# Performance work log

Hardware: AMD Instinct MI355X
Metric: run time of the kernel (lower is better)

## Reference

```python
import jax, jax.numpy as jnp
import numpy as np
import math

B, S, D = 2, 2048, 2048
H, HK = 32, 8          # query heads, kv heads
HD = D // H            # 64
REP = H // HK          # 4


def setup_inputs() -> dict:
    key = jax.random.key(0)
    ks = jax.random.split(key, 6)
    x = jax.random.normal(ks[0], (B, S, D), jnp.float32)
    # RoPE tables, rotate_half convention: halves duplicated along last dim
    inv_freq = 1.0 / (10000.0 ** (jnp.arange(0, HD, 2, dtype=jnp.float32) / HD))
    freqs = jnp.arange(S, dtype=jnp.float32)[:, None] * inv_freq[None, :]  # [S, HD/2]
    cos = jnp.concatenate([jnp.cos(freqs), jnp.cos(freqs)], axis=-1)       # [S, HD]
    sin = jnp.concatenate([jnp.sin(freqs), jnp.sin(freqs)], axis=-1)
    attn_mask = jnp.tril(jnp.ones((S, S), dtype=bool))
    std = 1.0 / math.sqrt(D)
    wq = jax.random.normal(ks[1], (D, D), jnp.float32) * std
    wk = jax.random.normal(ks[2], (HK * HD, D), jnp.float32) * std
    wv = jax.random.normal(ks[3], (HK * HD, D), jnp.float32) * std
    wo = jax.random.normal(ks[4], (D, D), jnp.float32) * std
    return {"x": x, "cos": cos, "sin": sin, "attn_mask": attn_mask,
            "wq": wq, "wk": wk, "wv": wv, "wo": wo}


def _rotate_half(t):
    h = t.shape[-1] // 2
    return jnp.concatenate([-t[..., h:], t[..., :h]], axis=-1)


def reference(x, cos, sin, attn_mask, wq, wk, wv, wo):
    b, s, d = x.shape
    q = (x @ wq.T).reshape(b, s, H, HD).transpose(0, 2, 1, 3)    # [b,H,s,hd]
    k = (x @ wk.T).reshape(b, s, HK, HD).transpose(0, 2, 1, 3)   # [b,HK,s,hd]
    v = (x @ wv.T).reshape(b, s, HK, HD).transpose(0, 2, 1, 3)
    c = cos[:s][None, None]
    sn = sin[:s][None, None]
    q = q * c + _rotate_half(q) * sn
    k = k * c + _rotate_half(k) * sn
    # GQA: group query heads instead of repeat_interleave'ing KV
    # repeat_interleave order == reshape (HK, REP): heads [g*REP : (g+1)*REP] share kv group g
    qg = q.reshape(b, HK, REP, s, HD)
    scores = jnp.einsum('bgrsd,bgtd->bgrst', qg, k) / math.sqrt(HD)  # [b,HK,REP,s,s]
    m = attn_mask[None, None, None, :, :]
    scores = jnp.where(m, scores, -jnp.inf)
    attn = jax.nn.softmax(scores, axis=-1)
    out = jnp.einsum('bgrst,bgtd->bgrsd', attn, v)                  # [b,HK,REP,s,hd]
    out = out.reshape(b, H, s, HD).transpose(0, 2, 1, 3).reshape(b, s, d)
    return out @ wo.T
```

## Files before the change

kernel.cpp:

```cpp
#include <hip/hip_runtime.h>
#include <hip/hip_bf16.h>
#include <math.h>

typedef __hip_bfloat16 bf16;
typedef __attribute__((ext_vector_type(8))) short bf16x8;
typedef __attribute__((ext_vector_type(4))) short short4v;
typedef __attribute__((ext_vector_type(4))) float f32x4;

static constexpr int B = 2, S = 2048, D = 2048, H = 32, HK = 8, HD = 64;
static constexpr int M = B * S;
static constexpr int NKV = HK * HD;
static constexpr int QKV3 = D + 2 * NKV;
static constexpr float SCALE2 = 0.125f * 1.44269504f;

__device__ __forceinline__ short bfbits(float x) {
  bf16 h = __float2bfloat16(x);
  return *reinterpret_cast<short*>(&h);
}

__device__ __forceinline__ void gl_lds16(const bf16* gp, bf16* lp) {
  __builtin_amdgcn_global_load_lds(
      (const __attribute__((address_space(1))) unsigned int*)(const void*)gp,
      (__attribute__((address_space(3))) unsigned int*)(void*)lp, 16, 0, 0);
}

struct alignas(8) bf4 { bf16 v[4]; };
static constexpr int N4_X  = M * D / 4;
static constexpr int N4_WQ = D * D / 4;
static constexpr int N4_WK = NKV * D / 4;
static constexpr int E0 = N4_X;
static constexpr int E1 = E0 + N4_WQ;
static constexpr int E2 = E1 + N4_WK;
static constexpr int E3 = E2 + N4_WK;
static constexpr int E4 = E3 + N4_WQ;
__global__ __launch_bounds__(256) void cast_all_kernel(const float* __restrict__ x,
                                                       const float* __restrict__ wq,
                                                       const float* __restrict__ wk,
                                                       const float* __restrict__ wv,
                                                       const float* __restrict__ wo,
                                                       bf16* __restrict__ xb,
                                                       bf16* __restrict__ wqkv,
                                                       bf16* __restrict__ wob) {
  int i = blockIdx.x * 256 + threadIdx.x;
  int stride = gridDim.x * 256;
  for (; i < E4; i += stride) {
    const float* s; bf16* d; int j;
    if (i < E0)      { s = x;  d = xb;   j = i; }
    else if (i < E1) { s = wq; d = wqkv; j = i - E0; }
    else if (i < E2) { s = wk; d = wqkv + (size_t)N4_WQ * 4; j = i - E1; }
    else if (i < E3) { s = wv; d = wqkv + (size_t)(N4_WQ + N4_WK) * 4; j = i - E2; }
    else             { s = wo; d = wob;  j = i - E3; }
    float4 f = reinterpret_cast<const float4*>(s)[j];
    bf4 o;
    o.v[0] = __float2bfloat16(f.x);
    o.v[1] = __float2bfloat16(f.y);
    o.v[2] = __float2bfloat16(f.z);
    o.v[3] = __float2bfloat16(f.w);
    reinterpret_cast<bf4*>(d)[j] = o;
  }
}

template <bool OUT_F32>
__global__ __launch_bounds__(256) void gemm_bt_kernel(const bf16* __restrict__ A,
                                                      const bf16* __restrict__ Bt,
                                                      void* __restrict__ C,
                                                      int Ndim, int Kdim) {
  __shared__ __align__(16) bf16 As[128][64];
  __shared__ __align__(16) bf16 Bs[128][64];
  const int tid = threadIdx.x;
  const int lane = tid & 63;
  const int w = tid >> 6;
  const int wm = w >> 1, wn = w & 1;
  const int r16 = lane & 15, g = lane >> 4;
  const int bm = blockIdx.y, bn = blockIdx.x;
  f32x4 acc[4][4] = {};

  const int nk = Kdim >> 6;
  for (int kt = 0; kt < nk; ++kt) {
    __syncthreads();
#pragma unroll
    for (int i = 0; i < 4; ++i) {
      int u = tid + i * 256;
      int rr = u >> 3, c8 = u & 7;
      int c8s = c8 ^ (rr & 7);
      gl_lds16(&A[(size_t)(bm * 128 + rr) * Kdim + kt * 64 + c8s * 8], &As[0][0] + (size_t)u * 8);
      gl_lds16(&Bt[(size_t)(bn * 128 + rr) * Kdim + kt * 64 + c8s * 8], &Bs[0][0] + (size_t)u * 8);
    }
    __syncthreads();
#pragma unroll
    for (int kc = 0; kc < 2; ++kc) {
      bf16x8 af[4], bfr[4];
      const int kq = kc * 4 + g;
#pragma unroll
      for (int m = 0; m < 4; ++m) {
        int ra = wm * 64 + m * 16 + r16;
        af[m] = *reinterpret_cast<const bf16x8*>(&As[ra][(kq ^ (ra & 7)) * 8]);
        int rb = wn * 64 + m * 16 + r16;
        bfr[m] = *reinterpret_cast<const bf16x8*>(&Bs[rb][(kq ^ (rb & 7)) * 8]);
      }
#pragma unroll
      for (int m = 0; m < 4; ++m)
#pragma unroll
        for (int n = 0; n < 4; ++n)
          acc[m][n] = __builtin_amdgcn_mfma_f32_16x16x32_bf16(af[m], bfr[n], acc[m][n], 0, 0, 0);
    }
  }
  const int row0 = bm * 128 + wm * 64 + g * 4;
  const int col0 = bn * 128 + wn * 64 + r16;
#pragma unroll
  for (int m = 0; m < 4; ++m)
#pragma unroll
    for (int n = 0; n < 4; ++n)
#pragma unroll
      for (int j = 0; j < 4; ++j) {
        size_t idx = (size_t)(row0 + m * 16 + j) * Ndim + col0 + n * 16;
        if (OUT_F32)
          reinterpret_cast<float*>(C)[idx] = acc[m][n][j];
        else
          reinterpret_cast<bf16*>(C)[idx] = __float2bfloat16(acc[m][n][j]);
      }
}

__global__ __launch_bounds__(256) void rope_kernel(bf16* __restrict__ t,
                                                   const float* __restrict__ cosb,
                                                   const float* __restrict__ sinb) {
  int idx = blockIdx.x * 256 + threadIdx.x;
  int i = idx & 31;
  int rest = idx >> 5;
  int hh = rest % 40;
  int s = (rest / 40) % S;
  int b = rest / (40 * S);
  size_t base = ((size_t)b * S + s) * QKV3 + hh * HD;
  float x0 = __bfloat162float(t[base + i]);
  float x1 = __bfloat162float(t[base + i + 32]);
  float c = cosb[s * HD + i];
  float sn = sinb[s * HD + i];
  float sc = (hh < 32) ? SCALE2 : 1.0f;
  t[base + i] = __float2bfloat16((x0 * c - x1 * sn) * sc);
  t[base + i + 32] = __float2bfloat16((x1 * c + x0 * sn) * sc);
}

__global__ __launch_bounds__(256) void transpose_v_kernel(const bf16* __restrict__ qkv,
                                                          bf16* __restrict__ vt) {
  __shared__ bf16 tile[64][65];
  const int st = blockIdx.x;
  const int bk = blockIdx.y;
  const int b = bk >> 3, hk = bk & 7;
  const int tid = threadIdx.x;
#pragma unroll
  for (int i = 0; i < 16; ++i) {
    int idx = tid + i * 256;
    int rs = idx >> 6, c = idx & 63;
    tile[rs][c] = qkv[((size_t)b * S + st * 64 + rs) * QKV3 + (D + NKV) + hk * HD + c];
  }
  __syncthreads();
#pragma unroll
  for (int i = 0; i < 16; ++i) {
    int idx = tid + i * 256;
    int rh = idx >> 6, cs = idx & 63;
    int blk = cs >> 5, kvl = cs & 31;
    int pos = ((kvl >> 2) & 3) * 8 + ((kvl >> 4) << 2) + (kvl & 3);
    vt[(((size_t)b * HK + hk) * HD + rh) * S + st * 64 + blk * 32 + pos] = tile[cs][rh];
  }
}

__global__ __launch_bounds__(256, 2) void attn_kernel(const bf16* __restrict__ qkv,
                                                      const bf16* __restrict__ vt,
                                                      bf16* __restrict__ ao) {
  __shared__ __align__(16) bf16 Ksh[2][64 * 64];
  __shared__ __align__(16) bf16 Vsh[2][64 * 64];
  const int u = blockIdx.x;
  const int y = blockIdx.y;
  const int b = y >> 3, hk = y & 7;
  const int tid = threadIdx.x;
  const int w = tid >> 6;
  const int h = hk * 4 + w;
  const int lane = tid & 63;
  const int r = lane & 15, g = lane >> 4;

  const bf16* qp  = qkv + ((size_t)b * S) * QKV3 + h * HD;
  const bf16* kvp = qkv + ((size_t)b * S) * QKV3 + D + hk * HD;
  const bf16* vtp = vt + (((size_t)b * HK + hk) * HD) * S;
  const int srow = tid >> 3;
  const int sc8 = tid & 7;

  bf16x8 ones;
#pragma unroll
  for (int j = 0; j < 8; ++j) ones[j] = (short)0x3F80;

  auto stage = [&](int buf, int kv0) {
#pragma unroll
    for (int i = 0; i < 2; ++i) {
      int rr = srow + i * 32;
      int cs = sc8 ^ (rr & 7);
      gl_lds16(&kvp[(size_t)(kv0 + rr) * QKV3 + cs * 8], &Ksh[buf][((size_t)rr * 8 + sc8) * 8]);
    }
#pragma unroll
    for (int i = 0; i < 2; ++i) {
      int rr = srow + i * 32;
      int cs = sc8 ^ (rr & 7);
      gl_lds16(&vtp[(size_t)rr * S + kv0 + cs * 8], &Vsh[buf][((size_t)rr * 8 + sc8) * 8]);
    }
  };

  for (int pass = 0; pass < 2; ++pass) {
    const int qb = pass ? (2016 - u * 32) : (u * 32);
    bf16x8 qfr[2][2];
#pragma unroll
    for (int qq = 0; qq < 2; ++qq)
#pragma unroll
      for (int hc = 0; hc < 2; ++hc)
        qfr[qq][hc] = *reinterpret_cast<const bf16x8*>(
            &qp[(size_t)(qb + qq * 16 + r) * QKV3 + hc * 32 + g * 8]);

    f32x4 o[4][2] = {};
    f32x4 ol[2] = {};
    const int kv_end = qb + 32;
    const int nch = (kv_end + 63) >> 6;

    stage(0, 0);
    __syncthreads();
    for (int c = 0; c < nch; ++c) {
      const int cur = c & 1;
      const int kv0 = c * 64;
      const bool lastc = (c == nch - 1);
      if (!lastc) stage(cur ^ 1, kv0 + 64);
      f32x4 scv[4][2] = {};
      __builtin_amdgcn_s_setprio(1);
#pragma unroll
      for (int f = 0; f < 4; ++f) {
        const int row = f * 16 + r;
#pragma unroll
        for (int hc = 0; hc < 2; ++hc) {
          bf16x8 kf = *reinterpret_cast<const bf16x8*>(
              &Ksh[cur][(size_t)row * 64 + (((hc * 4 + g) ^ (r & 7)) * 8)]);
          scv[f][0] = __builtin_amdgcn_mfma_f32_16x16x32_bf16(kf, qfr[0][hc], scv[f][0], 0, 0, 0);
          scv[f][1] = __builtin_amdgcn_mfma_f32_16x16x32_bf16(kf, qfr[1][hc], scv[f][1], 0, 0, 0);
        }
      }
      __builtin_amdgcn_s_setprio(0);
      if (lastc) {
#pragma unroll
        for (int qq = 0; qq < 2; ++qq) {
          const int qi = qb + qq * 16 + r;
#pragma unroll
          for (int f = 0; f < 4; ++f)
#pragma unroll
            for (int j = 0; j < 4; ++j)
              if (kv0 + f * 16 + g * 4 + j > qi) scv[f][qq][j] = -1e30f;
        }
      }
#pragma unroll
      for (int blk = 0; blk < 2; ++blk) {
        bf16x8 pb0, pb1;
#pragma unroll
        for (int jj = 0; jj < 8; ++jj) {
          const int f = blk * 2 + (jj >> 2), j = jj & 3;
          pb0[jj] = bfbits(exp2f(scv[f][0][j]));
          pb1[jj] = bfbits(exp2f(scv[f][1][j]));
        }
        __builtin_amdgcn_s_setprio(1);
        ol[0] = __builtin_amdgcn_mfma_f32_16x16x32_bf16(ones, pb0, ol[0], 0, 0, 0);
        ol[1] = __builtin_amdgcn_mfma_f32_16x16x32_bf16(ones, pb1, ol[1], 0, 0, 0);
#pragma unroll
        for (int d = 0; d < 4; ++d) {
          bf16x8 vf = *reinterpret_cast<const bf16x8*>(
              &Vsh[cur][(size_t)(d * 16 + r) * 64 + (((blk * 4 + g) ^ (r & 7)) * 8)]);
          o[d][0] = __builtin_amdgcn_mfma_f32_16x16x32_bf16(vf, pb0, o[d][0], 0, 0, 0);
          o[d][1] = __builtin_amdgcn_mfma_f32_16x16x32_bf16(vf, pb1, o[d][1], 0, 0, 0);
        }
        __builtin_amdgcn_s_setprio(0);
      }
      __syncthreads();
    }
#pragma unroll
    for (int qq = 0; qq < 2; ++qq) {
      float inv = 1.0f / ol[qq][0];
#pragma unroll
      for (int d = 0; d < 4; ++d) {
        short4v ov;
        ov[0] = bfbits(o[d][qq][0] * inv);
        ov[1] = bfbits(o[d][qq][1] * inv);
        ov[2] = bfbits(o[d][qq][2] * inv);
        ov[3] = bfbits(o[d][qq][3] * inv);
        *reinterpret_cast<short4v*>(
            &ao[(((size_t)b * S + qb + qq * 16 + r) * H + h) * HD + d * 16 + g * 4]) = ov;
      }
    }
  }
}

extern "C" void kernel_launch(void* const* d_in, const int* in_sizes, int n_in,
                              void* d_out, int out_size, void* d_ws, size_t ws_size,
                              hipStream_t stream) {
  (void)in_sizes; (void)n_in; (void)out_size; (void)ws_size;
  const float* x    = (const float*)d_in[0];
  const float* cosb = (const float*)d_in[1];
  const float* sinb = (const float*)d_in[2];
  const float* wq   = (const float*)d_in[4];
  const float* wk   = (const float*)d_in[5];
  const float* wv   = (const float*)d_in[6];
  const float* wo   = (const float*)d_in[7];

  char* ws = (char*)d_ws;
  size_t off = 0;
  auto alloc = [&](size_t elems) {
    bf16* p = (bf16*)(ws + off);
    off = (off + elems * sizeof(bf16) + 255) & ~(size_t)255;
    return p;
  };
  bf16* xb    = alloc((size_t)M * D);
  bf16* wqkvb = alloc((size_t)QKV3 * D);
  bf16* wob   = alloc((size_t)D * D);
  bf16* qkvb  = alloc((size_t)M * QKV3);
  bf16* vtb   = alloc((size_t)B * HK * HD * S);
  bf16* aob   = alloc((size_t)M * D);

  cast_all_kernel<<<dim3(2048), dim3(256), 0, stream>>>(x, wq, wk, wv, wo, xb, wqkvb, wob);

  gemm_bt_kernel<false><<<dim3(QKV3 / 128, M / 128), 256, 0, stream>>>(xb, wqkvb, qkvb, QKV3, D);

  rope_kernel<<<dim3(B * S * 40 * 32 / 256), 256, 0, stream>>>(qkvb, cosb, sinb);

  transpose_v_kernel<<<dim3(S / 64, B * HK), 256, 0, stream>>>(qkvb, vtb);

  attn_kernel<<<dim3(32, B * HK), 256, 0, stream>>>(qkvb, vtb, aob);

  gemm_bt_kernel<true><<<dim3(D / 128, M / 128), 256, 0, stream>>>(aob, wob, d_out, D, D);
}
```

Measured before the change: 198.2 us.

## Fuse Q RoPE into attention and stage two KV tiles per barrier

Q RoPE and softmax scaling are now applied inside the attention kernel when Q fragments are loaded, so the standalone rope kernel only rotates K heads and no longer reads and writes the large Q slice. The attention main loop now stages 128 KV rows (two 64-row tiles) per iteration into a quadruple-buffered LDS layout, which halves the number of block barriers. The cost is double the LDS footprint (64 KB per block), which may limit occupancy against the two blocks per CU the launch bounds request.

```diff
diff --git a/kernel.cpp b/kernel.cpp
--- a/kernel.cpp
+++ b/kernel.cpp
@@ -16,6 +16,11 @@
 __device__ __forceinline__ short bfbits(float x) {
   bf16 h = __float2bfloat16(x);
   return *reinterpret_cast<short*>(&h);
+}
+
+__device__ __forceinline__ float bf2f(short bits) {
+  unsigned int u = ((unsigned int)(unsigned short)bits) << 16;
+  return __builtin_bit_cast(float, u);
 }
 
 __device__ __forceinline__ void gl_lds16(const bf16* gp, bf16* lp) {
@@ -121,23 +126,22 @@
       }
 }
 
-__global__ __launch_bounds__(256) void rope_kernel(bf16* __restrict__ t,
-                                                   const float* __restrict__ cosb,
-                                                   const float* __restrict__ sinb) {
+__global__ __launch_bounds__(256) void rope_k_kernel(bf16* __restrict__ t,
+                                                     const float* __restrict__ cosb,
+                                                     const float* __restrict__ sinb) {
   int idx = blockIdx.x * 256 + threadIdx.x;
   int i = idx & 31;
   int rest = idx >> 5;
-  int hh = rest % 40;
-  int s = (rest / 40) % S;
-  int b = rest / (40 * S);
-  size_t base = ((size_t)b * S + s) * QKV3 + hh * HD;
+  int hh = rest & 7;
+  int s = (rest >> 3) % S;
+  int b = rest / (8 * S);
+  size_t base = ((size_t)b * S + s) * QKV3 + D + hh * HD;
   float x0 = __bfloat162float(t[base + i]);
   float x1 = __bfloat162float(t[base + i + 32]);
   float c = cosb[s * HD + i];
   float sn = sinb[s * HD + i];
-  float sc = (hh < 32) ? SCALE2 : 1.0f;
-  t[base + i] = __float2bfloat16((x0 * c - x1 * sn) * sc);
-  t[base + i + 32] = __float2bfloat16((x1 * c + x0 * sn) * sc);
+  t[base + i] = __float2bfloat16(x0 * c - x1 * sn);
+  t[base + i + 32] = __float2bfloat16(x1 * c + x0 * sn);
 }
 
 __global__ __launch_bounds__(256) void transpose_v_kernel(const bf16* __restrict__ qkv,
@@ -166,9 +170,11 @@
 
 __global__ __launch_bounds__(256, 2) void attn_kernel(const bf16* __restrict__ qkv,
                                                       const bf16* __restrict__ vt,
+                                                      const float* __restrict__ cosb,
+                                                      const float* __restrict__ sinb,
                                                       bf16* __restrict__ ao) {
-  __shared__ __align__(16) bf16 Ksh[2][64 * 64];
-  __shared__ __align__(16) bf16 Vsh[2][64 * 64];
+  __shared__ __align__(16) bf16 Ksh[4][64 * 64];
+  __shared__ __align__(16) bf16 Vsh[4][64 * 64];
   const int u = blockIdx.x;
   const int y = blockIdx.y;
   const int b = y >> 3, hk = y & 7;
@@ -188,18 +194,18 @@
 #pragma unroll
   for (int j = 0; j < 8; ++j) ones[j] = (short)0x3F80;
 
-  auto stage = [&](int buf, int kv0) {
+  auto stage64 = [&](int tl, int kv0) {
 #pragma unroll
     for (int i = 0; i < 2; ++i) {
       int rr = srow + i * 32;
       int cs = sc8 ^ (rr & 7);
-      gl_lds16(&kvp[(size_t)(kv0 + rr) * QKV3 + cs * 8], &Ksh[buf][((size_t)rr * 8 + sc8) * 8]);
+      gl_lds16(&kvp[(size_t)(kv0 + rr) * QKV3 + cs * 8], &Ksh[tl][((size_t)rr * 8 + sc8) * 8]);
     }
 #pragma unroll
     for (int i = 0; i < 2; ++i) {
       int rr = srow + i * 32;
       int cs = sc8 ^ (rr & 7);
-      gl_lds16(&vtp[(size_t)rr * S + kv0 + cs * 8], &Vsh[buf][((size_t)rr * 8 + sc8) * 8]);
+      gl_lds16(&vtp[(size_t)rr * S + kv0 + cs * 8], &Vsh[tl][((size_t)rr * 8 + sc8) * 8]);
     }
   };
 
@@ -207,69 +213,91 @@
     const int qb = pass ? (2016 - u * 32) : (u * 32);
     bf16x8 qfr[2][2];
 #pragma unroll
-    for (int qq = 0; qq < 2; ++qq)
-#pragma unroll
-      for (int hc = 0; hc < 2; ++hc)
-        qfr[qq][hc] = *reinterpret_cast<const bf16x8*>(
-            &qp[(size_t)(qb + qq * 16 + r) * QKV3 + hc * 32 + g * 8]);
+    for (int qq = 0; qq < 2; ++qq) {
+      const int srowq = qb + qq * 16 + r;
+      bf16x8 f0 = *reinterpret_cast<const bf16x8*>(&qp[(size_t)srowq * QKV3 + g * 8]);
+      bf16x8 f1 = *reinterpret_cast<const bf16x8*>(&qp[(size_t)srowq * QKV3 + 32 + g * 8]);
+      float4 c0 = reinterpret_cast<const float4*>(&cosb[(size_t)srowq * HD + g * 8])[0];
+      float4 c1 = reinterpret_cast<const float4*>(&cosb[(size_t)srowq * HD + g * 8])[1];
+      float4 s0 = reinterpret_cast<const float4*>(&sinb[(size_t)srowq * HD + g * 8])[0];
+      float4 s1 = reinterpret_cast<const float4*>(&sinb[(size_t)srowq * HD + g * 8])[1];
+      float cc[8] = {c0.x, c0.y, c0.z, c0.w, c1.x, c1.y, c1.z, c1.w};
+      float ss[8] = {s0.x, s0.y, s0.z, s0.w, s1.x, s1.y, s1.z, s1.w};
+#pragma unroll
+      for (int j = 0; j < 8; ++j) {
+        float x0 = bf2f(f0[j]), x1 = bf2f(f1[j]);
+        qfr[qq][0][j] = bfbits((x0 * cc[j] - x1 * ss[j]) * SCALE2);
+        qfr[qq][1][j] = bfbits((x1 * cc[j] + x0 * ss[j]) * SCALE2);
+      }
+    }
 
     f32x4 o[4][2] = {};
     f32x4 ol[2] = {};
     const int kv_end = qb + 32;
-    const int nch = (kv_end + 63) >> 6;
-
-    stage(0, 0);
+    const int nch = (kv_end + 127) >> 7;
+
+    stage64(0, 0);
+    stage64(1, 64);
     __syncthreads();
     for (int c = 0; c < nch; ++c) {
-      const int cur = c & 1;
-      const int kv0 = c * 64;
-      const bool lastc = (c == nch - 1);
-      if (!lastc) stage(cur ^ 1, kv0 + 64);
-      f32x4 scv[4][2] = {};
-      __builtin_amdgcn_s_setprio(1);
-#pragma unroll
-      for (int f = 0; f < 4; ++f) {
-        const int row = f * 16 + r;
-#pragma unroll
-        for (int hc = 0; hc < 2; ++hc) {
-          bf16x8 kf = *reinterpret_cast<const bf16x8*>(
-              &Ksh[cur][(size_t)row * 64 + (((hc * 4 + g) ^ (r & 7)) * 8)]);
-          scv[f][0] = __builtin_amdgcn_mfma_f32_16x16x32_bf16(kf, qfr[0][hc], scv[f][0], 0, 0, 0);
-          scv[f][1] = __builtin_amdgcn_mfma_f32_16x16x32_bf16(kf, qfr[1][hc], scv[f][1], 0, 0, 0);
-        }
-      }
-      __builtin_amdgcn_s_setprio(0);
-      if (lastc) {
-#pragma unroll
-        for (int qq = 0; qq < 2; ++qq) {
-          const int qi = qb + qq * 16 + r;
-#pragma unroll
-          for (int f = 0; f < 4; ++f)
-#pragma unroll
-            for (int j = 0; j < 4; ++j)
-              if (kv0 + f * 16 + g * 4 + j > qi) scv[f][qq][j] = -1e30f;
-        }
-      }
-#pragma unroll
-      for (int blk = 0; blk < 2; ++blk) {
-        bf16x8 pb0, pb1;
-#pragma unroll
-        for (int jj = 0; jj < 8; ++jj) {
-          const int f = blk * 2 + (jj >> 2), j = jj & 3;
-          pb0[jj] = bfbits(exp2f(scv[f][0][j]));
-          pb1[jj] = bfbits(exp2f(scv[f][1][j]));
-        }
+      const int base_t = (c & 1) * 2;
+      if (c + 1 < nch) {
+        const int nb = ((c + 1) & 1) * 2;
+        stage64(nb, (c + 1) * 128);
+        stage64(nb + 1, (c + 1) * 128 + 64);
+      }
+#pragma unroll
+      for (int t = 0; t < 2; ++t) {
+        const int kv0 = c * 128 + t * 64;
+        if (kv0 >= kv_end) break;
+        const int tl = base_t + t;
+        const bool lasth = (kv0 + 64 >= kv_end);
+        f32x4 scv[4][2] = {};
         __builtin_amdgcn_s_setprio(1);
-        ol[0] = __builtin_amdgcn_mfma_f32_16x16x32_bf16(ones, pb0, ol[0], 0, 0, 0);
-        ol[1] = __builtin_amdgcn_mfma_f32_16x16x32_bf16(ones, pb1, ol[1], 0, 0, 0);
-#pragma unroll
-        for (int d = 0; d < 4; ++d) {
-          bf16x8 vf = *reinterpret_cast<const bf16x8*>(
-              &Vsh[cur][(size_t)(d * 16 + r) * 64 + (((blk * 4 + g) ^ (r & 7)) * 8)]);
-          o[d][0] = __builtin_amdgcn_mfma_f32_16x16x32_bf16(vf, pb0, o[d][0], 0, 0, 0);
-          o[d][1] = __builtin_amdgcn_mfma_f32_16x16x32_bf16(vf, pb1, o[d][1], 0, 0, 0);
+#pragma unroll
+        for (int f = 0; f < 4; ++f) {
+          const int row = f * 16 + r;
+#pragma unroll
+          for (int hc = 0; hc < 2; ++hc) {
+            bf16x8 kf = *reinterpret_cast<const bf16x8*>(
+                &Ksh[tl][(size_t)row * 64 + (((hc * 4 + g) ^ (r & 7)) * 8)]);
+            scv[f][0] = __builtin_amdgcn_mfma_f32_16x16x32_bf16(kf, qfr[0][hc], scv[f][0], 0, 0, 0);
+            scv[f][1] = __builtin_amdgcn_mfma_f32_16x16x32_bf16(kf, qfr[1][hc], scv[f][1], 0, 0, 0);
+          }
         }
         __builtin_amdgcn_s_setprio(0);
+        if (lasth) {
+#pragma unroll
+          for (int qq = 0; qq < 2; ++qq) {
+            const int qi = qb + qq * 16 + r;
+#pragma unroll
+            for (int f = 0; f < 4; ++f)
+#pragma unroll
+              for (int j = 0; j < 4; ++j)
+                if (kv0 + f * 16 + g * 4 + j > qi) scv[f][qq][j] = -1e30f;
+          }
+        }
+#pragma unroll
+        for (int blk = 0; blk < 2; ++blk) {
+          bf16x8 pb0, pb1;
+#pragma unroll
+          for (int jj = 0; jj < 8; ++jj) {
+            const int f = blk * 2 + (jj >> 2), j = jj & 3;
+            pb0[jj] = bfbits(exp2f(scv[f][0][j]));
+            pb1[jj] = bfbits(exp2f(scv[f][1][j]));
+          }
+          __builtin_amdgcn_s_setprio(1);
+          ol[0] = __builtin_amdgcn_mfma_f32_16x16x32_bf16(ones, pb0, ol[0], 0, 0, 0);
+          ol[1] = __builtin_amdgcn_mfma_f32_16x16x32_bf16(ones, pb1, ol[1], 0, 0, 0);
+#pragma unroll
+          for (int d = 0; d < 4; ++d) {
+            bf16x8 vf = *reinterpret_cast<const bf16x8*>(
+                &Vsh[tl][(size_t)(d * 16 + r) * 64 + (((blk * 4 + g) ^ (r & 7)) * 8)]);
+            o[d][0] = __builtin_amdgcn_mfma_f32_16x16x32_bf16(vf, pb0, o[d][0], 0, 0, 0);
+            o[d][1] = __builtin_amdgcn_mfma_f32_16x16x32_bf16(vf, pb1, o[d][1], 0, 0, 0);
+          }
+          __builtin_amdgcn_s_setprio(0);
+        }
       }
       __syncthreads();
     }
@@ -320,11 +348,11 @@
 
   gemm_bt_kernel<false><<<dim3(QKV3 / 128, M / 128), 256, 0, stream>>>(xb, wqkvb, qkvb, QKV3, D);
 
-  rope_kernel<<<dim3(B * S * 40 * 32 / 256), 256, 0, stream>>>(qkvb, cosb, sinb);
+  rope_k_kernel<<<dim3(B * S * 8 * 32 / 256), 256, 0, stream>>>(qkvb, cosb, sinb);
 
   transpose_v_kernel<<<dim3(S / 64, B * HK), 256, 0, stream>>>(qkvb, vtb);
 
-  attn_kernel<<<dim3(32, B * HK), 256, 0, stream>>>(qkvb, vtb, aob);
+  attn_kernel<<<dim3(32, B * HK), 256, 0, stream>>>(qkvb, vtb, cosb, sinb, aob);
 
   gemm_bt_kernel<true><<<dim3(D / 128, M / 128), 256, 0, stream>>>(aob, wob, d_out, D, D);
 }
```

Measured after the change: 190.3 us. 4.0% less time.

## Fuse Q RoPE into attention and halve query tile to double grid

Applied to the files above, without the earlier changes.

Applies rotary embedding and softmax scaling to Q inside the attention kernel while loading fragments, so the standalone rope pass now touches only K heads. Each block now handles 16 query rows per pass instead of 32, the grid doubles to 64 blocks per (batch, kv head), and launch bounds ask for 4 blocks per SM. The goal is to cut rope memory traffic and raise occupancy and parallelism. The cost is that each K/V chunk loaded into LDS is reused by half as many queries, so K/V traffic per query doubles.

```diff
diff --git a/kernel.cpp b/kernel.cpp
--- a/kernel.cpp
+++ b/kernel.cpp
@@ -16,6 +16,11 @@
 __device__ __forceinline__ short bfbits(float x) {
   bf16 h = __float2bfloat16(x);
   return *reinterpret_cast<short*>(&h);
+}
+
+__device__ __forceinline__ float bf2f(short bits) {
+  unsigned int u = ((unsigned int)(unsigned short)bits) << 16;
+  return __builtin_bit_cast(float, u);
 }
 
 __device__ __forceinline__ void gl_lds16(const bf16* gp, bf16* lp) {
@@ -121,23 +126,22 @@
       }
 }
 
-__global__ __launch_bounds__(256) void rope_kernel(bf16* __restrict__ t,
-                                                   const float* __restrict__ cosb,
-                                                   const float* __restrict__ sinb) {
+__global__ __launch_bounds__(256) void rope_k_kernel(bf16* __restrict__ t,
+                                                     const float* __restrict__ cosb,
+                                                     const float* __restrict__ sinb) {
   int idx = blockIdx.x * 256 + threadIdx.x;
   int i = idx & 31;
   int rest = idx >> 5;
-  int hh = rest % 40;
-  int s = (rest / 40) % S;
-  int b = rest / (40 * S);
-  size_t base = ((size_t)b * S + s) * QKV3 + hh * HD;
+  int hh = rest & 7;
+  int s = (rest >> 3) % S;
+  int b = rest / (8 * S);
+  size_t base = ((size_t)b * S + s) * QKV3 + D + hh * HD;
   float x0 = __bfloat162float(t[base + i]);
   float x1 = __bfloat162float(t[base + i + 32]);
   float c = cosb[s * HD + i];
   float sn = sinb[s * HD + i];
-  float sc = (hh < 32) ? SCALE2 : 1.0f;
-  t[base + i] = __float2bfloat16((x0 * c - x1 * sn) * sc);
-  t[base + i + 32] = __float2bfloat16((x1 * c + x0 * sn) * sc);
+  t[base + i] = __float2bfloat16(x0 * c - x1 * sn);
+  t[base + i + 32] = __float2bfloat16(x1 * c + x0 * sn);
 }
 
 __global__ __launch_bounds__(256) void transpose_v_kernel(const bf16* __restrict__ qkv,
@@ -164,8 +168,10 @@
   }
 }
 
-__global__ __launch_bounds__(256, 2) void attn_kernel(const bf16* __restrict__ qkv,
+__global__ __launch_bounds__(256, 4) void attn_kernel(const bf16* __restrict__ qkv,
                                                       const bf16* __restrict__ vt,
+                                                      const float* __restrict__ cosb,
+                                                      const float* __restrict__ sinb,
                                                       bf16* __restrict__ ao) {
   __shared__ __align__(16) bf16 Ksh[2][64 * 64];
   __shared__ __align__(16) bf16 Vsh[2][64 * 64];
@@ -188,7 +194,7 @@
 #pragma unroll
   for (int j = 0; j < 8; ++j) ones[j] = (short)0x3F80;
 
-  auto stage = [&](int buf, int kv0) {
+  auto stage64 = [&](int buf, int kv0) {
 #pragma unroll
     for (int i = 0; i < 2; ++i) {
       int rr = srow + i * 32;
@@ -204,28 +210,39 @@
   };
 
   for (int pass = 0; pass < 2; ++pass) {
-    const int qb = pass ? (2016 - u * 32) : (u * 32);
-    bf16x8 qfr[2][2];
-#pragma unroll
-    for (int qq = 0; qq < 2; ++qq)
-#pragma unroll
-      for (int hc = 0; hc < 2; ++hc)
-        qfr[qq][hc] = *reinterpret_cast<const bf16x8*>(
-            &qp[(size_t)(qb + qq * 16 + r) * QKV3 + hc * 32 + g * 8]);
-
-    f32x4 o[4][2] = {};
-    f32x4 ol[2] = {};
-    const int kv_end = qb + 32;
+    const int qb = pass ? (2032 - u * 16) : (u * 16);
+    const int qi = qb + r;
+    bf16x8 qfr[2];
+    {
+      bf16x8 f0 = *reinterpret_cast<const bf16x8*>(&qp[(size_t)qi * QKV3 + g * 8]);
+      bf16x8 f1 = *reinterpret_cast<const bf16x8*>(&qp[(size_t)qi * QKV3 + 32 + g * 8]);
+      float4 c0 = reinterpret_cast<const float4*>(&cosb[(size_t)qi * HD + g * 8])[0];
+      float4 c1 = reinterpret_cast<const float4*>(&cosb[(size_t)qi * HD + g * 8])[1];
+      float4 s0 = reinterpret_cast<const float4*>(&sinb[(size_t)qi * HD + g * 8])[0];
+      float4 s1 = reinterpret_cast<const float4*>(&sinb[(size_t)qi * HD + g * 8])[1];
+      float cc[8] = {c0.x, c0.y, c0.z, c0.w, c1.x, c1.y, c1.z, c1.w};
+      float ss[8] = {s0.x, s0.y, s0.z, s0.w, s1.x, s1.y, s1.z, s1.w};
+#pragma unroll
+      for (int j = 0; j < 8; ++j) {
+        float x0 = bf2f(f0[j]), x1 = bf2f(f1[j]);
+        qfr[0][j] = bfbits((x0 * cc[j] - x1 * ss[j]) * SCALE2);
+        qfr[1][j] = bfbits((x1 * cc[j] + x0 * ss[j]) * SCALE2);
+      }
+    }
+
+    f32x4 o[4] = {};
+    f32x4 ol = {};
+    const int kv_end = qb + 16;
     const int nch = (kv_end + 63) >> 6;
 
-    stage(0, 0);
+    stage64(0, 0);
     __syncthreads();
     for (int c = 0; c < nch; ++c) {
       const int cur = c & 1;
       const int kv0 = c * 64;
       const bool lastc = (c == nch - 1);
-      if (!lastc) stage(cur ^ 1, kv0 + 64);
-      f32x4 scv[4][2] = {};
+      if (!lastc) stage64(cur ^ 1, kv0 + 64);
+      f32x4 scv[4] = {};
       __builtin_amdgcn_s_setprio(1);
 #pragma unroll
       for (int f = 0; f < 4; ++f) {
@@ -234,57 +251,48 @@
         for (int hc = 0; hc < 2; ++hc) {
           bf16x8 kf = *reinterpret_cast<const bf16x8*>(
               &Ksh[cur][(size_t)row * 64 + (((hc * 4 + g) ^ (r & 7)) * 8)]);
-          scv[f][0] = __builtin_amdgcn_mfma_f32_16x16x32_bf16(kf, qfr[0][hc], scv[f][0], 0, 0, 0);
-          scv[f][1] = __builtin_amdgcn_mfma_f32_16x16x32_bf16(kf, qfr[1][hc], scv[f][1], 0, 0, 0);
+          scv[f] = __builtin_amdgcn_mfma_f32_16x16x32_bf16(kf, qfr[hc], scv[f], 0, 0, 0);
         }
       }
       __builtin_amdgcn_s_setprio(0);
       if (lastc) {
 #pragma unroll
-        for (int qq = 0; qq < 2; ++qq) {
-          const int qi = qb + qq * 16 + r;
-#pragma unroll
-          for (int f = 0; f < 4; ++f)
-#pragma unroll
-            for (int j = 0; j < 4; ++j)
-              if (kv0 + f * 16 + g * 4 + j > qi) scv[f][qq][j] = -1e30f;
-        }
+        for (int f = 0; f < 4; ++f)
+#pragma unroll
+          for (int j = 0; j < 4; ++j)
+            if (kv0 + f * 16 + g * 4 + j > qi) scv[f][j] = -1e30f;
       }
 #pragma unroll
       for (int blk = 0; blk < 2; ++blk) {
-        bf16x8 pb0, pb1;
+        bf16x8 pb;
 #pragma unroll
         for (int jj = 0; jj < 8; ++jj) {
           const int f = blk * 2 + (jj >> 2), j = jj & 3;
-          pb0[jj] = bfbits(exp2f(scv[f][0][j]));
-          pb1[jj] = bfbits(exp2f(scv[f][1][j]));
+          pb[jj] = bfbits(exp2f(scv[f][j]));
         }
         __builtin_amdgcn_s_setprio(1);
-        ol[0] = __builtin_amdgcn_mfma_f32_16x16x32_bf16(ones, pb0, ol[0], 0, 0, 0);
-        ol[1] = __builtin_amdgcn_mfma_f32_16x16x32_bf16(ones, pb1, ol[1], 0, 0, 0);
+        ol = __builtin_amdgcn_mfma_f32_16x16x32_bf16(ones, pb, ol, 0, 0, 0);
 #pragma unroll
         for (int d = 0; d < 4; ++d) {
           bf16x8 vf = *reinterpret_cast<const bf16x8*>(
               &Vsh[cur][(size_t)(d * 16 + r) * 64 + (((blk * 4 + g) ^ (r & 7)) * 8)]);
-          o[d][0] = __builtin_amdgcn_mfma_f32_16x16x32_bf16(vf, pb0, o[d][0], 0, 0, 0);
-          o[d][1] = __builtin_amdgcn_mfma_f32_16x16x32_bf16(vf, pb1, o[d][1], 0, 0, 0);
+          o[d] = __builtin_amdgcn_mfma_f32_16x16x32_bf16(vf, pb, o[d], 0, 0, 0);
         }
         __builtin_amdgcn_s_setprio(0);
       }
       __syncthreads();
     }
-#pragma unroll
-    for (int qq = 0; qq < 2; ++qq) {
-      float inv = 1.0f / ol[qq][0];
+    {
+      float inv = 1.0f / ol[0];
 #pragma unroll
       for (int d = 0; d < 4; ++d) {
         short4v ov;
-        ov[0] = bfbits(o[d][qq][0] * inv);
-        ov[1] = bfbits(o[d][qq][1] * inv);
-        ov[2] = bfbits(o[d][qq][2] * inv);
-        ov[3] = bfbits(o[d][qq][3] * inv);
+        ov[0] = bfbits(o[d][0] * inv);
+        ov[1] = bfbits(o[d][1] * inv);
+        ov[2] = bfbits(o[d][2] * inv);
+        ov[3] = bfbits(o[d][3] * inv);
         *reinterpret_cast<short4v*>(
-            &ao[(((size_t)b * S + qb + qq * 16 + r) * H + h) * HD + d * 16 + g * 4]) = ov;
+            &ao[(((size_t)b * S + qi) * H + h) * HD + d * 16 + g * 4]) = ov;
       }
     }
   }
@@ -320,11 +328,11 @@
 
   gemm_bt_kernel<false><<<dim3(QKV3 / 128, M / 128), 256, 0, stream>>>(xb, wqkvb, qkvb, QKV3, D);
 
-  rope_kernel<<<dim3(B * S * 40 * 32 / 256), 256, 0, stream>>>(qkvb, cosb, sinb);
+  rope_k_kernel<<<dim3(B * S * 8 * 32 / 256), 256, 0, stream>>>(qkvb, cosb, sinb);
 
   transpose_v_kernel<<<dim3(S / 64, B * HK), 256, 0, stream>>>(qkvb, vtb);
 
-  attn_kernel<<<dim3(32, B * HK), 256, 0, stream>>>(qkvb, vtb, aob);
+  attn_kernel<<<dim3(64, B * HK), 256, 0, stream>>>(qkvb, vtb, cosb, sinb, aob);
 
   gemm_bt_kernel<true><<<dim3(D / 128, M / 128), 256, 0, stream>>>(aob, wob, d_out, D, D);
 }
```

After: 191.8 us. 1.03x faster.
